# Kernel optimization log

Hardware: AMD Instinct MI355X
Metric: run time of the kernel (lower is better)

The kernel has to match this reference:

```python
import jax, jax.numpy as jnp
import numpy as np

DECAY = 0.99
EPS = 1e-12  # torch F.normalize eps


def setup_inputs() -> dict:
    key = jax.random.key(0)
    ks = jax.random.split(key, 5)
    B, S, H, M = 4, 4096, 1024, 256
    x = jax.random.normal(ks[0], (B, S, H), dtype=jnp.float32)
    Wq = jax.random.normal(ks[1], (M, H), dtype=jnp.float32) * (H ** -0.5)
    Wk = jax.random.normal(ks[2], (M, H), dtype=jnp.float32) * (H ** -0.5)
    Wv = jax.random.normal(ks[3], (M, H), dtype=jnp.float32) * (H ** -0.5)
    # original inits W_out to zeros; use small random weights so the baseline output is non-trivial
    Wo = jax.random.normal(ks[4], (H, M), dtype=jnp.float32) * (M ** -0.5)
    M0 = jnp.zeros((M, M), dtype=jnp.float32)
    return {"x": x, "Wq": Wq, "Wk": Wk, "Wv": Wv, "Wo": Wo, "M0": M0, "chunk_size": 64}


def _l2norm(t):
    return t / jnp.maximum(jnp.linalg.norm(t, axis=-1, keepdims=True), EPS)


def reference(x, Wq, Wk, Wv, Wo, M0, chunk_size):
    B, S, H = x.shape
    m = Wq.shape[0]
    q = jnp.einsum('bsh,mh->bsm', x, Wq)
    k = _l2norm(jnp.einsum('bsh,mh->bsm', x, Wk))
    v = _l2norm(jnp.einsum('bsh,mh->bsm', x, Wv))
    n_chunks = S // chunk_size
    # (n_chunks, B, c, m)
    qc = q.reshape(B, n_chunks, chunk_size, m).transpose(1, 0, 2, 3)
    kc = k.reshape(B, n_chunks, chunk_size, m).transpose(1, 0, 2, 3)
    vc = v.reshape(B, n_chunks, chunk_size, m).transpose(1, 0, 2, 3)
    decay_c = DECAY ** chunk_size
    scale = 1.0 / (B * chunk_size)

    def step(M, qkv):
        qch, kch, vch = qkv
        r = jnp.einsum('bcm,nm->bcn', qch, M)  # q @ M.T
        outer = jnp.einsum('bci,bcj->ij', vch, kch) * scale
        return decay_c * M + outer, r

    _, rs = jax.lax.scan(step, M0, (qc, kc, vc))  # rs: (n_chunks, B, c, m)
    retrieved = rs.transpose(1, 0, 2, 3).reshape(B, S, m)
    return jnp.einsum('bsm,hm->bsh', retrieved, Wo)
```

## Files before the change

### kernel.cpp

```cpp
#include <hip/hip_runtime.h>
#include <math.h>

#define BB 4
#define SS 4096
#define HH 1024
#define MM 256
#define CHUNK 64
#define NCHUNK 64
#define ROWS (BB*SS)
#define QKV_LD 768
#define DECAY_F 0.99

typedef unsigned short u16;
typedef __attribute__((ext_vector_type(8))) short bf16x8;
typedef __attribute__((ext_vector_type(8))) unsigned short u16x8;
typedef __attribute__((ext_vector_type(4))) float f32x4;

__device__ inline u16 f2b(float f) {
  union { float f; unsigned u; } v; v.f = f;
  unsigned r = v.u + 0x7FFF + ((v.u >> 16) & 1);
  return (u16)(r >> 16);
}
__device__ inline float b2f(u16 h) {
  union { unsigned u; float f; } v; v.u = ((unsigned)h) << 16; return v.f;
}

__device__ inline void gload16(const void* g, void* l) {
  __builtin_amdgcn_global_load_lds(
      (const __attribute__((address_space(1))) unsigned int*)g,
      (__attribute__((address_space(3))) unsigned int*)l, 16, 0, 0);
}

__global__ __launch_bounds__(256) void cast_x_kernel(const float* __restrict__ src,
                                                     u16* __restrict__ dst) {
  int i = blockIdx.x * 256 + threadIdx.x;
  float4 v = reinterpret_cast<const float4*>(src)[i];
  ushort4 o;
  o.x = f2b(v.x); o.y = f2b(v.y); o.z = f2b(v.z); o.w = f2b(v.w);
  reinterpret_cast<ushort4*>(dst)[i] = o;
}

__global__ __launch_bounds__(256) void cast_w_kernel(const float* __restrict__ Wq,
                                                     const float* __restrict__ Wk,
                                                     const float* __restrict__ Wv,
                                                     const float* __restrict__ Wo,
                                                     u16* __restrict__ Wqkv_b,
                                                     u16* __restrict__ Wo_b) {
  int b = blockIdx.x, which = b >> 8;
  int i = ((b & 255) << 8) + threadIdx.x;
  const float* src = which == 0 ? Wq : which == 1 ? Wk : which == 2 ? Wv : Wo;
  u16* dst = which < 3 ? Wqkv_b + which * (MM * HH) : Wo_b;
  float4 v = reinterpret_cast<const float4*>(src)[i];
  ushort4 o;
  o.x = f2b(v.x); o.y = f2b(v.y); o.z = f2b(v.z); o.w = f2b(v.w);
  reinterpret_cast<ushort4*>(dst)[i] = o;
}

template<int OUT_BF16>
__global__ __launch_bounds__(512, 2) void gemm256(const u16* __restrict__ A,
                                                  const u16* __restrict__ B,
                                                  void* __restrict__ Cv,
                                                  int K, int lda, int ldb, int ldc) {
  __shared__ bf16x8 LD[2][2][2][16][64];
  const int tid = threadIdx.x, lane = tid & 63, wv = tid >> 6;
  const int wr = wv >> 2, wc = wv & 3;

  const int gx = gridDim.x;
  const int nwg = gx * gridDim.y;
  const int lin = blockIdx.y * gx + blockIdx.x;
  const int chunk = nwg >> 3;
  const int orig = (lin & 7) * chunk + (lin >> 3);
  const int bx = orig % gx, by = orig / gx;
  const int row0 = by * 256, col0 = bx * 256;
  const int NT = K >> 6;

  const int fr = lane & 15;
  const int kg = (lane >> 4) << 3;

  auto stage2 = [&](int kt, int db, int part) {
    const int ab = part >> 1;
    const int j = part & 1;
    const int tile = wv + (j << 3);
    const u16* base = ab ? B : A;
    const int ld = ab ? ldb : lda;
    const int rc0 = ab ? col0 : row0;
    const u16* g = base + (size_t)(rc0 + tile * 16 + fr) * ld + kt * 64 + kg;
    gload16(g,      &LD[db][ab][0][tile][0]);
    gload16(g + 32, &LD[db][ab][1][tile][0]);
  };

  bf16x8 aq[4][2], bq[4][2];
  auto readAquad = [&](int db, int h) {
#pragma unroll
    for (int i = 0; i < 4; ++i)
#pragma unroll
      for (int s = 0; s < 2; ++s)
        aq[i][s] = LD[db][0][s][wr * 8 + h * 4 + i][lane];
  };
  auto readB2 = [&](int db, int nh) {
#pragma unroll
    for (int j = 0; j < 2; ++j)
#pragma unroll
      for (int s = 0; s < 2; ++s)
        bq[nh * 2 + j][s] = LD[db][1][s][wc * 4 + nh * 2 + j][lane];
  };

  f32x4 acc[8][4] = {};
  auto cluster = [&](int h, int nh) {
#pragma unroll
    for (int i = 0; i < 4; ++i)
#pragma unroll
      for (int j = 0; j < 2; ++j)
#pragma unroll
        for (int s = 0; s < 2; ++s)
          acc[h * 4 + i][nh * 2 + j] = __builtin_amdgcn_mfma_f32_16x16x32_bf16(
              aq[i][s], bq[nh * 2 + j][s], acc[h * 4 + i][nh * 2 + j], 0, 0, 0);
  };

  stage2(0, 0, 0); stage2(0, 0, 1); stage2(0, 0, 2); stage2(0, 0, 3);

  for (int kt = 0; kt < NT; ++kt) {
    const int db = kt & 1;
    const bool pf = (kt + 1 < NT);
    if (pf) stage2(kt + 1, db ^ 1, 0);
    if (pf) asm volatile("s_waitcnt vmcnt(2)" ::: "memory");
    else    asm volatile("s_waitcnt vmcnt(0)" ::: "memory");
    __builtin_amdgcn_s_barrier();
    asm volatile("" ::: "memory");
    readAquad(db, 0);
    readB2(db, 0);
    __builtin_amdgcn_s_setprio(1); cluster(0, 0); __builtin_amdgcn_s_setprio(0);
    __builtin_amdgcn_s_barrier();
    readB2(db, 1);
    if (pf) stage2(kt + 1, db ^ 1, 1);
    __builtin_amdgcn_s_barrier();
    __builtin_amdgcn_s_setprio(1); cluster(0, 1); __builtin_amdgcn_s_setprio(0);
    __builtin_amdgcn_s_barrier();
    readAquad(db, 1);
    if (pf) stage2(kt + 1, db ^ 1, 2);
    __builtin_amdgcn_s_barrier();
    __builtin_amdgcn_s_setprio(1); cluster(1, 0); __builtin_amdgcn_s_setprio(0);
    __builtin_amdgcn_s_barrier();
    if (pf) stage2(kt + 1, db ^ 1, 3);
    __builtin_amdgcn_s_barrier();
    __builtin_amdgcn_s_setprio(1); cluster(1, 1); __builtin_amdgcn_s_setprio(0);
    __builtin_amdgcn_s_barrier();
  }

  const int r4 = (lane >> 4) << 2;
  const int cc = lane & 15;
#pragma unroll
  for (int mi = 0; mi < 8; ++mi)
#pragma unroll
    for (int nj = 0; nj < 4; ++nj)
#pragma unroll
      for (int r = 0; r < 4; ++r) {
        int lr = wr * 128 + mi * 16 + r4 + r;
        int lc = wc * 64 + nj * 16 + cc;
        float vv = acc[mi][nj][r];
        if (OUT_BF16) ((u16*)Cv)[(size_t)(row0 + lr) * ldc + col0 + lc] = f2b(vv);
        else          ((float*)Cv)[(size_t)(row0 + lr) * ldc + col0 + lc] = vv;
      }
}

#define M_OUTER 2
#define M_RETR  3

template<int MODE>
__global__ __launch_bounds__(256) void gemm128(const u16* __restrict__ A,
                                               const u16* __restrict__ Bg,
                                               void* __restrict__ Cv,
                                               int K, int lda, int ldb,
                                               float scale) {
  __shared__ bf16x8 As[3][512];
  __shared__ bf16x8 Bs[3][512];
  const int tid = threadIdx.x, lane = tid & 63, wv = tid >> 6;
  const int wr = wv >> 1, wc = wv & 1;
  const int t = blockIdx.z;
  const int bx = blockIdx.x, by = blockIdx.y;
  const int row0 = by * 128;
  const int col0 = bx * 128;
  const int NK = K >> 5;
  const u16* Bbase = (MODE == M_RETR) ? (Bg + (size_t)t * (MM * MM)) : Bg;

  auto stage = [&](int ks, int buf) {
    int koff;
    if (MODE == M_OUTER) koff = ((ks >> 1) << 12) + t * CHUNK + ((ks & 1) << 5);
    else                 koff = ks << 5;
#pragma unroll
    for (int j = 0; j < 2; ++j) {
      int m = j * 4 + wv;
      int rf = m * 16 + (lane & 15);
      size_t arow;
      if (MODE == M_RETR)
        arow = (size_t)(2 * by + (rf >> 6)) * SS + (size_t)t * CHUNK + (rf & 63);
      else
        arow = (size_t)(row0 + rf);
      const u16* ga = A + arow * (size_t)lda + koff + ((lane >> 4) << 3);
      gload16(ga, &As[buf][m * 64]);
      const u16* gb = Bbase + (size_t)(col0 + rf) * ldb + koff + ((lane >> 4) << 3);
      gload16(gb, &Bs[buf][m * 64]);
    }
  };

  f32x4 acc[4][4] = {};
  stage(0, 0);
  stage(1, 1);
  int rb = 0, sb = 2;
  for (int ks = 0; ks < NK; ++ks) {
    if (ks + 1 < NK) asm volatile("s_waitcnt vmcnt(4)" ::: "memory");
    else             asm volatile("s_waitcnt vmcnt(0)" ::: "memory");
    __builtin_amdgcn_s_barrier();
    asm volatile("" ::: "memory");
    if (ks + 2 < NK) stage(ks + 2, sb);
    bf16x8 af[4], bfr[4];
#pragma unroll
    for (int m = 0; m < 4; ++m) af[m] = As[rb][(wr * 4 + m) * 64 + lane];
#pragma unroll
    for (int n = 0; n < 4; ++n) bfr[n] = Bs[rb][(wc * 4 + n) * 64 + lane];
#pragma unroll
    for (int m = 0; m < 4; ++m)
#pragma unroll
      for (int n = 0; n < 4; ++n)
        acc[m][n] = __builtin_amdgcn_mfma_f32_16x16x32_bf16(af[m], bfr[n], acc[m][n], 0, 0, 0);
    rb = (rb == 2) ? 0 : rb + 1;
    sb = (sb == 2) ? 0 : sb + 1;
  }

  const int r4 = (lane >> 4) << 2;
  const int cc = lane & 15;
#pragma unroll
  for (int m = 0; m < 4; ++m)
#pragma unroll
    for (int n = 0; n < 4; ++n)
#pragma unroll
      for (int r = 0; r < 4; ++r) {
        int lr = wr * 64 + m * 16 + r4 + r;
        int lc = wc * 64 + n * 16 + cc;
        float vv = acc[m][n][r];
        if (MODE == M_OUTER) {
          ((float*)Cv)[(size_t)t * (MM * MM) + (size_t)(row0 + lr) * MM + col0 + lc] = vv * scale;
        } else {
          size_t rowg = (size_t)(2 * by + (lr >> 6)) * SS + (size_t)t * CHUNK + (lr & 63);
          ((u16*)Cv)[rowg * MM + col0 + lc] = f2b(vv);
        }
      }
}

__global__ __launch_bounds__(256) void l2normT_kernel(const u16* __restrict__ qkv,
                                                      u16* __restrict__ kT,
                                                      u16* __restrict__ vT) {
  __shared__ u16 T[256][72];
  __shared__ float ps[64][4];
  __shared__ float inv[64];
  const int tid = threadIdx.x;
  const int q = tid >> 6, rl = tid & 63;
  const int row0 = blockIdx.x * 64;
#pragma unroll 1
  for (int seg = 0; seg < 2; ++seg) {
    u16* dstT = seg ? vT : kT;
    const int segbase = 256 + seg * 256;
    float ss = 0.f;
#pragma unroll
    for (int i = 0; i < 8; ++i) {
      u16x8 v = *reinterpret_cast<const u16x8*>(
          qkv + (size_t)(row0 + rl) * QKV_LD + segbase + q * 64 + i * 8);
#pragma unroll
      for (int e = 0; e < 8; ++e) {
        float f = b2f(v[e]);
        ss += f * f;
        T[q * 64 + i * 8 + e][rl] = v[e];
      }
    }
    ps[rl][q] = ss;
    __syncthreads();
    if (tid < 64) {
      float s = ps[tid][0] + ps[tid][1] + ps[tid][2] + ps[tid][3];
      inv[tid] = 1.0f / fmaxf(sqrtf(s), 1e-12f);
    }
    __syncthreads();
#pragma unroll
    for (int p = 0; p < 8; ++p) {
      int c = p * 32 + q * 8 + (rl >> 3);
      int r0 = (rl & 7) * 8;
      u16x8 val = *reinterpret_cast<const u16x8*>(&T[c][r0]);
      u16x8 o;
#pragma unroll
      for (int e = 0; e < 8; ++e) o[e] = f2b(b2f(val[e]) * inv[r0 + e]);
      *reinterpret_cast<u16x8*>(dstT + (size_t)c * ROWS + row0 + r0) = o;
    }
    __syncthreads();
  }
}

__global__ __launch_bounds__(256) void prefix_kernel(const float* __restrict__ outer,
                                                     const float* __restrict__ M0,
                                                     u16* __restrict__ Mprev_b,
                                                     float decay_c) {
  int ij = blockIdx.x * 256 + threadIdx.x;
  float run = M0[ij];
  float pre[8];
#pragma unroll
  for (int d = 0; d < 8; ++d) pre[d] = outer[(size_t)d * (MM * MM) + ij];
#pragma unroll 1
  for (int tb = 0; tb < NCHUNK; tb += 8) {
#pragma unroll
    for (int d = 0; d < 8; ++d) {
      int tc = tb + d;
      float o = pre[d];
      if (tb + 8 < NCHUNK) pre[d] = outer[(size_t)(tc + 8) * (MM * MM) + ij];
      Mprev_b[(size_t)tc * (MM * MM) + ij] = f2b(run);
      run = decay_c * run + o;
    }
  }
}

extern "C" void kernel_launch(void* const* d_in, const int* in_sizes, int n_in,
                              void* d_out, int out_size, void* d_ws, size_t ws_size,
                              hipStream_t stream) {
  const float* x  = (const float*)d_in[0];
  const float* Wq = (const float*)d_in[1];
  const float* Wk = (const float*)d_in[2];
  const float* Wv = (const float*)d_in[3];
  const float* Wo = (const float*)d_in[4];
  const float* M0 = (const float*)d_in[5];
  float* out = (float*)d_out;

  char* ws = (char*)d_ws;
  u16*   xb      = (u16*)(ws);
  u16*   qkv_b   = (u16*)(ws + 33554432);
  u16*   Wqkv_b  = (u16*)(ws + 58720256);
  u16*   Wo_b    = (u16*)(ws + 60293120);
  u16*   kT      = (u16*)(ws);
  u16*   vT      = (u16*)(ws + 8388608);
  float* outer   = (float*)(ws + 16777216);
  u16*   Mprev_b = (u16*)(ws);
  u16*   r_b     = (u16*)(ws + 8388608);

  const float scale   = 1.0f / (BB * CHUNK);
  const float decay_c = (float)pow(DECAY_F, (double)CHUNK);
  dim3 blk(256), blk512(512);

  cast_x_kernel<<<(ROWS * HH / 4) / 256, blk, 0, stream>>>(x, xb);
  cast_w_kernel<<<1024, blk, 0, stream>>>(Wq, Wk, Wv, Wo, Wqkv_b, Wo_b);
  gemm256<1><<<dim3(QKV_LD / 256, ROWS / 256), blk512, 0, stream>>>(
      xb, Wqkv_b, qkv_b, HH, HH, HH, QKV_LD);
  l2normT_kernel<<<ROWS / 64, blk, 0, stream>>>(qkv_b, kT, vT);
  gemm128<M_OUTER><<<dim3(2, 2, NCHUNK), blk, 0, stream>>>(
      vT, kT, outer, MM, ROWS, ROWS, scale);
  prefix_kernel<<<(MM * MM) / 256, blk, 0, stream>>>(outer, M0, Mprev_b, decay_c);
  gemm128<M_RETR><<<dim3(2, 2, NCHUNK), blk, 0, stream>>>(
      qkv_b, Mprev_b, r_b, MM, QKV_LD, MM, 0.f);
  gemm256<0><<<dim3(HH / 256, ROWS / 256), blk512, 0, stream>>>(
      r_b, Wo_b, out, MM, MM, MM, HH);
}
```

Baseline: 140.5 us.

## Fuse fp32-to-bf16 cast of x into QKV GEMM A-tile loading

Removes the separate cast_x kernel and has the QKV GEMM read x in fp32, convert it to bf16 in registers and write it to LDS inside the pipelined main loop. The QKV GEMM tile also changes to 256x192 (12 B tiles, 4x64 grid), so the 768 output columns split over four blocks instead of three. This drops a full bf16 round trip of x through memory (write plus reread). In exchange A loads go through registers instead of direct-to-LDS, which adds VGPR pressure, and x is read as fp32 once per column block, now four times instead of three.

```diff
diff --git a/kernel.cpp b/kernel.cpp
--- a/kernel.cpp
+++ b/kernel.cpp
@@ -24,20 +24,17 @@
 __device__ inline float b2f(u16 h) {
   union { unsigned u; float f; } v; v.u = ((unsigned)h) << 16; return v.f;
 }
+__device__ inline u16x8 cvt8(float4 p, float4 q) {
+  u16x8 h;
+  h[0] = f2b(p.x); h[1] = f2b(p.y); h[2] = f2b(p.z); h[3] = f2b(p.w);
+  h[4] = f2b(q.x); h[5] = f2b(q.y); h[6] = f2b(q.z); h[7] = f2b(q.w);
+  return h;
+}
 
 __device__ inline void gload16(const void* g, void* l) {
   __builtin_amdgcn_global_load_lds(
       (const __attribute__((address_space(1))) unsigned int*)g,
       (__attribute__((address_space(3))) unsigned int*)l, 16, 0, 0);
-}
-
-__global__ __launch_bounds__(256) void cast_x_kernel(const float* __restrict__ src,
-                                                     u16* __restrict__ dst) {
-  int i = blockIdx.x * 256 + threadIdx.x;
-  float4 v = reinterpret_cast<const float4*>(src)[i];
-  ushort4 o;
-  o.x = f2b(v.x); o.y = f2b(v.y); o.z = f2b(v.z); o.w = f2b(v.w);
-  reinterpret_cast<ushort4*>(dst)[i] = o;
 }
 
 __global__ __launch_bounds__(256) void cast_w_kernel(const float* __restrict__ Wq,
@@ -56,14 +53,17 @@
   reinterpret_cast<ushort4*>(dst)[i] = o;
 }
 
-template<int OUT_BF16>
-__global__ __launch_bounds__(512, 2) void gemm256(const u16* __restrict__ A,
+template<int NBT, int A_F32, int OUT_BF16>
+__global__ __launch_bounds__(512, 2) void gemm256(const void* __restrict__ Ap,
                                                   const u16* __restrict__ B,
                                                   void* __restrict__ Cv,
                                                   int K, int lda, int ldb, int ldc) {
-  __shared__ bf16x8 LD[2][2][2][16][64];
+  constexpr int NFR = NBT / 4;
+  __shared__ bf16x8 LA[2][2][16][64];
+  __shared__ bf16x8 LB[2][2][NBT][64];
   const int tid = threadIdx.x, lane = tid & 63, wv = tid >> 6;
   const int wr = wv >> 2, wc = wv & 3;
+  const int wvm3 = wv % 3;
 
   const int gx = gridDim.x;
   const int nwg = gx * gridDim.y;
@@ -71,77 +71,111 @@
   const int chunk = nwg >> 3;
   const int orig = (lin & 7) * chunk + (lin >> 3);
   const int bx = orig % gx, by = orig / gx;
-  const int row0 = by * 256, col0 = bx * 256;
+  const int row0 = by * 256, col0 = bx * (NBT * 16);
   const int NT = K >> 6;
 
   const int fr = lane & 15;
   const int kg = (lane >> 4) << 3;
 
-  auto stage2 = [&](int kt, int db, int part) {
-    const int ab = part >> 1;
-    const int j = part & 1;
-    const int tile = wv + (j << 3);
-    const u16* base = ab ? B : A;
-    const int ld = ab ? ldb : lda;
-    const int rc0 = ab ? col0 : row0;
-    const u16* g = base + (size_t)(rc0 + tile * 16 + fr) * ld + kt * 64 + kg;
-    gload16(g,      &LD[db][ab][0][tile][0]);
-    gload16(g + 32, &LD[db][ab][1][tile][0]);
-  };
-
-  bf16x8 aq[4][2], bq[4][2];
-  auto readAquad = [&](int db, int h) {
+  auto stageB = [&](int kt, int db_, int tile) {
+    const u16* g = B + (size_t)(col0 + tile * 16 + fr) * (size_t)ldb + kt * 64 + kg;
+    gload16(g,      &LB[db_][0][tile][0]);
+    gload16(g + 32, &LB[db_][1][tile][0]);
+  };
+  auto stageA_lds = [&](int kt, int db_, int tile) {
+    const u16* g = (const u16*)Ap + (size_t)(row0 + tile * 16 + fr) * (size_t)lda + kt * 64 + kg;
+    gload16(g,      &LA[db_][0][tile][0]);
+    gload16(g + 32, &LA[db_][1][tile][0]);
+  };
+  auto loadA = [&](int kt, int tile, float4& p0, float4& p1, float4& p2, float4& p3) {
+    const float* g = (const float*)Ap + (size_t)(row0 + tile * 16 + fr) * (size_t)lda + kt * 64 + kg;
+    p0 = *(const float4*)g;        p1 = *(const float4*)(g + 4);
+    p2 = *(const float4*)(g + 32); p3 = *(const float4*)(g + 36);
+  };
+  auto writeA = [&](int db_, int tile, float4 p0, float4 p1, float4 p2, float4 p3) {
+    *reinterpret_cast<u16x8*>(&LA[db_][0][tile][lane]) = cvt8(p0, p1);
+    *reinterpret_cast<u16x8*>(&LA[db_][1][tile][lane]) = cvt8(p2, p3);
+  };
+
+  bf16x8 aq[4][2], bq[NFR][2];
+  auto readAquad = [&](int db_, int h) {
 #pragma unroll
     for (int i = 0; i < 4; ++i)
 #pragma unroll
       for (int s = 0; s < 2; ++s)
-        aq[i][s] = LD[db][0][s][wr * 8 + h * 4 + i][lane];
-  };
-  auto readB2 = [&](int db, int nh) {
-#pragma unroll
-    for (int j = 0; j < 2; ++j)
+        aq[i][s] = LA[db_][s][wr * 8 + h * 4 + i][lane];
+  };
+  auto readBhalf = [&](int db_, int half) {
+    const int n0 = half ? 2 : 0, n1 = half ? NFR : 2;
+#pragma unroll
+    for (int n = n0; n < n1; ++n)
 #pragma unroll
       for (int s = 0; s < 2; ++s)
-        bq[nh * 2 + j][s] = LD[db][1][s][wc * 4 + nh * 2 + j][lane];
-  };
-
-  f32x4 acc[8][4] = {};
-  auto cluster = [&](int h, int nh) {
+        bq[n][s] = LB[db_][s][wc * NFR + n][lane];
+  };
+
+  f32x4 acc[8][NFR] = {};
+  auto cluster = [&](int h, int half) {
+    const int n0 = half ? 2 : 0, n1 = half ? NFR : 2;
 #pragma unroll
     for (int i = 0; i < 4; ++i)
 #pragma unroll
-      for (int j = 0; j < 2; ++j)
+      for (int n = n0; n < n1; ++n)
 #pragma unroll
         for (int s = 0; s < 2; ++s)
-          acc[h * 4 + i][nh * 2 + j] = __builtin_amdgcn_mfma_f32_16x16x32_bf16(
-              aq[i][s], bq[nh * 2 + j][s], acc[h * 4 + i][nh * 2 + j], 0, 0, 0);
-  };
-
-  stage2(0, 0, 0); stage2(0, 0, 1); stage2(0, 0, 2); stage2(0, 0, 3);
+          acc[h * 4 + i][n] = __builtin_amdgcn_mfma_f32_16x16x32_bf16(
+              aq[i][s], bq[n][s], acc[h * 4 + i][n], 0, 0, 0);
+  };
+
+  float4 pA0, pA1, pA2, pA3, pB0, pB1, pB2, pB3;
+
+  if constexpr (A_F32) {
+    stageB(0, 0, 0 + wvm3); stageB(0, 0, 3 + wvm3);
+    stageB(0, 0, 6 + wvm3); stageB(0, 0, 9 + wvm3);
+    loadA(0, wv,     pA0, pA1, pA2, pA3);
+    writeA(0, wv,    pA0, pA1, pA2, pA3);
+    loadA(0, wv + 8, pB0, pB1, pB2, pB3);
+    writeA(0, wv + 8, pB0, pB1, pB2, pB3);
+    asm volatile("s_waitcnt lgkmcnt(0)" ::: "memory");
+  } else {
+    stageA_lds(0, 0, wv); stageA_lds(0, 0, wv + 8);
+    stageB(0, 0, wv);     stageB(0, 0, wv + 8);
+  }
 
   for (int kt = 0; kt < NT; ++kt) {
-    const int db = kt & 1;
+    const int db = kt & 1, sb = db ^ 1;
     const bool pf = (kt + 1 < NT);
-    if (pf) stage2(kt + 1, db ^ 1, 0);
+    if (pf) { if constexpr (A_F32) stageB(kt + 1, sb, 0 + wvm3); else stageA_lds(kt + 1, sb, wv); }
     if (pf) asm volatile("s_waitcnt vmcnt(2)" ::: "memory");
     else    asm volatile("s_waitcnt vmcnt(0)" ::: "memory");
     __builtin_amdgcn_s_barrier();
     asm volatile("" ::: "memory");
     readAquad(db, 0);
-    readB2(db, 0);
+    readBhalf(db, 0);
     __builtin_amdgcn_s_setprio(1); cluster(0, 0); __builtin_amdgcn_s_setprio(0);
     __builtin_amdgcn_s_barrier();
-    readB2(db, 1);
-    if (pf) stage2(kt + 1, db ^ 1, 1);
+    readBhalf(db, 1);
+    if (pf) { if constexpr (A_F32) stageB(kt + 1, sb, 3 + wvm3); else stageA_lds(kt + 1, sb, wv + 8); }
     __builtin_amdgcn_s_barrier();
     __builtin_amdgcn_s_setprio(1); cluster(0, 1); __builtin_amdgcn_s_setprio(0);
     __builtin_amdgcn_s_barrier();
     readAquad(db, 1);
-    if (pf) stage2(kt + 1, db ^ 1, 2);
+    if (pf) {
+      if constexpr (A_F32) { loadA(kt + 1, wv, pA0, pA1, pA2, pA3); stageB(kt + 1, sb, 6 + wvm3); }
+      else stageB(kt + 1, sb, wv);
+    }
     __builtin_amdgcn_s_barrier();
     __builtin_amdgcn_s_setprio(1); cluster(1, 0); __builtin_amdgcn_s_setprio(0);
     __builtin_amdgcn_s_barrier();
-    if (pf) stage2(kt + 1, db ^ 1, 3);
+    if (pf) {
+      if constexpr (A_F32) {
+        writeA(sb, wv, pA0, pA1, pA2, pA3);
+        loadA(kt + 1, wv + 8, pB0, pB1, pB2, pB3);
+        stageB(kt + 1, sb, 9 + wvm3);
+        writeA(sb, wv + 8, pB0, pB1, pB2, pB3);
+        asm volatile("s_waitcnt lgkmcnt(0)" ::: "memory");
+      } else stageB(kt + 1, sb, wv + 8);
+    }
     __builtin_amdgcn_s_barrier();
     __builtin_amdgcn_s_setprio(1); cluster(1, 1); __builtin_amdgcn_s_setprio(0);
     __builtin_amdgcn_s_barrier();
@@ -152,11 +186,11 @@
 #pragma unroll
   for (int mi = 0; mi < 8; ++mi)
 #pragma unroll
-    for (int nj = 0; nj < 4; ++nj)
+    for (int nj = 0; nj < NFR; ++nj)
 #pragma unroll
       for (int r = 0; r < 4; ++r) {
         int lr = wr * 128 + mi * 16 + r4 + r;
-        int lc = wc * 64 + nj * 16 + cc;
+        int lc = wc * (NFR * 16) + nj * 16 + cc;
         float vv = acc[mi][nj][r];
         if (OUT_BF16) ((u16*)Cv)[(size_t)(row0 + lr) * ldc + col0 + lc] = f2b(vv);
         else          ((float*)Cv)[(size_t)(row0 + lr) * ldc + col0 + lc] = vv;
@@ -327,30 +361,28 @@
   float* out = (float*)d_out;
 
   char* ws = (char*)d_ws;
-  u16*   xb      = (u16*)(ws);
-  u16*   qkv_b   = (u16*)(ws + 33554432);
+  u16*   qkv_b   = (u16*)(ws);
+  u16*   kT      = (u16*)(ws + 25165824);
+  u16*   vT      = (u16*)(ws + 33554432);
+  float* outer   = (float*)(ws + 41943040);
+  u16*   Mprev_b = (u16*)(ws + 25165824);
+  u16*   r_b     = (u16*)(ws + 33554432);
   u16*   Wqkv_b  = (u16*)(ws + 58720256);
   u16*   Wo_b    = (u16*)(ws + 60293120);
-  u16*   kT      = (u16*)(ws);
-  u16*   vT      = (u16*)(ws + 8388608);
-  float* outer   = (float*)(ws + 16777216);
-  u16*   Mprev_b = (u16*)(ws);
-  u16*   r_b     = (u16*)(ws + 8388608);
 
   const float scale   = 1.0f / (BB * CHUNK);
   const float decay_c = (float)pow(DECAY_F, (double)CHUNK);
   dim3 blk(256), blk512(512);
 
-  cast_x_kernel<<<(ROWS * HH / 4) / 256, blk, 0, stream>>>(x, xb);
   cast_w_kernel<<<1024, blk, 0, stream>>>(Wq, Wk, Wv, Wo, Wqkv_b, Wo_b);
-  gemm256<1><<<dim3(QKV_LD / 256, ROWS / 256), blk512, 0, stream>>>(
-      xb, Wqkv_b, qkv_b, HH, HH, HH, QKV_LD);
+  gemm256<12, 1, 1><<<dim3(4, 64), blk512, 0, stream>>>(
+      x, Wqkv_b, qkv_b, HH, HH, HH, QKV_LD);
   l2normT_kernel<<<ROWS / 64, blk, 0, stream>>>(qkv_b, kT, vT);
   gemm128<M_OUTER><<<dim3(2, 2, NCHUNK), blk, 0, stream>>>(
       vT, kT, outer, MM, ROWS, ROWS, scale);
   prefix_kernel<<<(MM * MM) / 256, blk, 0, stream>>>(outer, M0, Mprev_b, decay_c);
   gemm128<M_RETR><<<dim3(2, 2, NCHUNK), blk, 0, stream>>>(
       qkv_b, Mprev_b, r_b, MM, QKV_LD, MM, 0.f);
-  gemm256<0><<<dim3(HH / 256, ROWS / 256), blk512, 0, stream>>>(
+  gemm256<16, 0, 0><<<dim3(4, 64), blk512, 0, stream>>>(
       r_b, Wo_b, out, MM, MM, MM, HH);
 }
```

Measured after the change: 164.1 us. 16.8% more time.

## Simplify GEMM pipeline to one barrier per k-tile with bulk prefetch

Applied to the files above, without the earlier changes.

Replaces the interleaved eight-barrier ping-pong schedule in the bf16 GEMM with a simpler loop. Each k-tile now waits for all loads, takes one barrier, issues every prefetch for the next tile, then reads all of B and A and runs the MFMA clusters back to back. This removes most barriers and the fine-grained staging. The trade-off is that global loads no longer interleave as tightly with compute, and the full vmcnt(0) wait can expose memory latency.

```diff
diff --git a/kernel.cpp b/kernel.cpp
--- a/kernel.cpp
+++ b/kernel.cpp
@@ -61,7 +61,8 @@
                                                   const u16* __restrict__ B,
                                                   void* __restrict__ Cv,
                                                   int K, int lda, int ldb, int ldc) {
-  __shared__ bf16x8 LD[2][2][2][16][64];
+  __shared__ bf16x8 LA[2][2][16][64];
+  __shared__ bf16x8 LB[2][2][16][64];
   const int tid = threadIdx.x, lane = tid & 63, wv = tid >> 6;
   const int wr = wv >> 2, wc = wv & 3;
 
@@ -77,32 +78,31 @@
   const int fr = lane & 15;
   const int kg = (lane >> 4) << 3;
 
-  auto stage2 = [&](int kt, int db, int part) {
-    const int ab = part >> 1;
-    const int j = part & 1;
-    const int tile = wv + (j << 3);
-    const u16* base = ab ? B : A;
-    const int ld = ab ? ldb : lda;
-    const int rc0 = ab ? col0 : row0;
-    const u16* g = base + (size_t)(rc0 + tile * 16 + fr) * ld + kt * 64 + kg;
-    gload16(g,      &LD[db][ab][0][tile][0]);
-    gload16(g + 32, &LD[db][ab][1][tile][0]);
+  auto stageA = [&](int kt, int db_, int tile) {
+    const u16* g = A + (size_t)(row0 + tile * 16 + fr) * (size_t)lda + kt * 64 + kg;
+    gload16(g,      &LA[db_][0][tile][0]);
+    gload16(g + 32, &LA[db_][1][tile][0]);
+  };
+  auto stageB = [&](int kt, int db_, int tile) {
+    const u16* g = B + (size_t)(col0 + tile * 16 + fr) * (size_t)ldb + kt * 64 + kg;
+    gload16(g,      &LB[db_][0][tile][0]);
+    gload16(g + 32, &LB[db_][1][tile][0]);
   };
 
   bf16x8 aq[4][2], bq[4][2];
-  auto readAquad = [&](int db, int h) {
+  auto readAquad = [&](int db_, int h) {
 #pragma unroll
     for (int i = 0; i < 4; ++i)
 #pragma unroll
       for (int s = 0; s < 2; ++s)
-        aq[i][s] = LD[db][0][s][wr * 8 + h * 4 + i][lane];
-  };
-  auto readB2 = [&](int db, int nh) {
-#pragma unroll
-    for (int j = 0; j < 2; ++j)
+        aq[i][s] = LA[db_][s][wr * 8 + h * 4 + i][lane];
+  };
+  auto readBall = [&](int db_) {
+#pragma unroll
+    for (int n = 0; n < 4; ++n)
 #pragma unroll
       for (int s = 0; s < 2; ++s)
-        bq[nh * 2 + j][s] = LD[db][1][s][wc * 4 + nh * 2 + j][lane];
+        bq[n][s] = LB[db_][s][wc * 4 + n][lane];
   };
 
   f32x4 acc[8][4] = {};
@@ -117,34 +117,27 @@
               aq[i][s], bq[nh * 2 + j][s], acc[h * 4 + i][nh * 2 + j], 0, 0, 0);
   };
 
-  stage2(0, 0, 0); stage2(0, 0, 1); stage2(0, 0, 2); stage2(0, 0, 3);
+  stageA(0, 0, wv); stageA(0, 0, wv + 8);
+  stageB(0, 0, wv); stageB(0, 0, wv + 8);
 
   for (int kt = 0; kt < NT; ++kt) {
-    const int db = kt & 1;
-    const bool pf = (kt + 1 < NT);
-    if (pf) stage2(kt + 1, db ^ 1, 0);
-    if (pf) asm volatile("s_waitcnt vmcnt(2)" ::: "memory");
-    else    asm volatile("s_waitcnt vmcnt(0)" ::: "memory");
+    const int db = kt & 1, sb = db ^ 1;
+    asm volatile("s_waitcnt vmcnt(0)" ::: "memory");
     __builtin_amdgcn_s_barrier();
     asm volatile("" ::: "memory");
+    if (kt + 1 < NT) {
+      stageA(kt + 1, sb, wv); stageA(kt + 1, sb, wv + 8);
+      stageB(kt + 1, sb, wv); stageB(kt + 1, sb, wv + 8);
+    }
     readAquad(db, 0);
-    readB2(db, 0);
-    __builtin_amdgcn_s_setprio(1); cluster(0, 0); __builtin_amdgcn_s_setprio(0);
-    __builtin_amdgcn_s_barrier();
-    readB2(db, 1);
-    if (pf) stage2(kt + 1, db ^ 1, 1);
-    __builtin_amdgcn_s_barrier();
-    __builtin_amdgcn_s_setprio(1); cluster(0, 1); __builtin_amdgcn_s_setprio(0);
-    __builtin_amdgcn_s_barrier();
+    readBall(db);
+    __builtin_amdgcn_s_setprio(1);
+    cluster(0, 0); cluster(0, 1);
+    __builtin_amdgcn_s_setprio(0);
     readAquad(db, 1);
-    if (pf) stage2(kt + 1, db ^ 1, 2);
-    __builtin_amdgcn_s_barrier();
-    __builtin_amdgcn_s_setprio(1); cluster(1, 0); __builtin_amdgcn_s_setprio(0);
-    __builtin_amdgcn_s_barrier();
-    if (pf) stage2(kt + 1, db ^ 1, 3);
-    __builtin_amdgcn_s_barrier();
-    __builtin_amdgcn_s_setprio(1); cluster(1, 1); __builtin_amdgcn_s_setprio(0);
-    __builtin_amdgcn_s_barrier();
+    __builtin_amdgcn_s_setprio(1);
+    cluster(1, 0); cluster(1, 1);
+    __builtin_amdgcn_s_setprio(0);
   }
 
   const int r4 = (lane >> 4) << 2;
```

Result: slower. 151.1 us (+7.6%).

## Fuse L2-normalize and transpose into QKV GEMM epilogue; merge cast kernels

Applied to the files above, without the earlier changes.

The QKV projection GEMM epilogue now writes q row-major and, for the k and v column tiles, computes row L2 norms by shuffle and shared-memory reduction, then writes normalized transposed kT/vT directly. This removes the separate l2normT kernel and the round trip of k and v through a bf16 qkv buffer. The two cast kernels are merged into one launch. The transposed epilogue stores are 8-byte strided writes, which may coalesce poorly, and the workspace layout is rearranged.

```diff
diff --git a/kernel.cpp b/kernel.cpp
--- a/kernel.cpp
+++ b/kernel.cpp
@@ -8,7 +8,6 @@
 #define CHUNK 64
 #define NCHUNK 64
 #define ROWS (BB*SS)
-#define QKV_LD 768
 #define DECAY_F 0.99
 
 typedef unsigned short u16;
@@ -31,35 +30,38 @@
       (__attribute__((address_space(3))) unsigned int*)l, 16, 0, 0);
 }
 
-__global__ __launch_bounds__(256) void cast_x_kernel(const float* __restrict__ src,
-                                                     u16* __restrict__ dst) {
-  int i = blockIdx.x * 256 + threadIdx.x;
+__global__ __launch_bounds__(256) void cast_all_kernel(const float* __restrict__ x,
+                                                       const float* __restrict__ Wq,
+                                                       const float* __restrict__ Wk,
+                                                       const float* __restrict__ Wv,
+                                                       const float* __restrict__ Wo,
+                                                       u16* __restrict__ xb,
+                                                       u16* __restrict__ Wqkv_b,
+                                                       u16* __restrict__ Wo_b) {
+  int b = blockIdx.x;
+  const float* src;
+  u16* dst;
+  int i;
+  if (b < 16384) {
+    src = x; dst = xb; i = (b << 8) + threadIdx.x;
+  } else {
+    int wb = b - 16384, which = wb >> 8;
+    i = ((wb & 255) << 8) + threadIdx.x;
+    src = which == 0 ? Wq : which == 1 ? Wk : which == 2 ? Wv : Wo;
+    dst = which < 3 ? Wqkv_b + which * (MM * HH) : Wo_b;
+  }
   float4 v = reinterpret_cast<const float4*>(src)[i];
   ushort4 o;
   o.x = f2b(v.x); o.y = f2b(v.y); o.z = f2b(v.z); o.w = f2b(v.w);
   reinterpret_cast<ushort4*>(dst)[i] = o;
 }
 
-__global__ __launch_bounds__(256) void cast_w_kernel(const float* __restrict__ Wq,
-                                                     const float* __restrict__ Wk,
-                                                     const float* __restrict__ Wv,
-                                                     const float* __restrict__ Wo,
-                                                     u16* __restrict__ Wqkv_b,
-                                                     u16* __restrict__ Wo_b) {
-  int b = blockIdx.x, which = b >> 8;
-  int i = ((b & 255) << 8) + threadIdx.x;
-  const float* src = which == 0 ? Wq : which == 1 ? Wk : which == 2 ? Wv : Wo;
-  u16* dst = which < 3 ? Wqkv_b + which * (MM * HH) : Wo_b;
-  float4 v = reinterpret_cast<const float4*>(src)[i];
-  ushort4 o;
-  o.x = f2b(v.x); o.y = f2b(v.y); o.z = f2b(v.z); o.w = f2b(v.w);
-  reinterpret_cast<ushort4*>(dst)[i] = o;
-}
-
-template<int OUT_BF16>
+template<int EPI>
 __global__ __launch_bounds__(512, 2) void gemm256(const u16* __restrict__ A,
                                                   const u16* __restrict__ B,
                                                   void* __restrict__ Cv,
+                                                  u16* __restrict__ kTd,
+                                                  u16* __restrict__ vTd,
                                                   int K, int lda, int ldb, int ldc) {
   __shared__ bf16x8 LD[2][2][2][16][64];
   const int tid = threadIdx.x, lane = tid & 63, wv = tid >> 6;
@@ -149,18 +151,76 @@
 
   const int r4 = (lane >> 4) << 2;
   const int cc = lane & 15;
-#pragma unroll
-  for (int mi = 0; mi < 8; ++mi)
-#pragma unroll
-    for (int nj = 0; nj < 4; ++nj)
-#pragma unroll
-      for (int r = 0; r < 4; ++r) {
-        int lr = wr * 128 + mi * 16 + r4 + r;
-        int lc = wc * 64 + nj * 16 + cc;
-        float vv = acc[mi][nj][r];
-        if (OUT_BF16) ((u16*)Cv)[(size_t)(row0 + lr) * ldc + col0 + lc] = f2b(vv);
-        else          ((float*)Cv)[(size_t)(row0 + lr) * ldc + col0 + lc] = vv;
+
+  if constexpr (EPI == 0) {
+#pragma unroll
+    for (int mi = 0; mi < 8; ++mi)
+#pragma unroll
+      for (int nj = 0; nj < 4; ++nj)
+#pragma unroll
+        for (int r = 0; r < 4; ++r) {
+          int lr = wr * 128 + mi * 16 + r4 + r;
+          int lc = wc * 64 + nj * 16 + cc;
+          ((float*)Cv)[(size_t)(row0 + lr) * ldc + col0 + lc] = acc[mi][nj][r];
+        }
+  } else {
+    if (bx == 0) {
+#pragma unroll
+      for (int mi = 0; mi < 8; ++mi)
+#pragma unroll
+        for (int nj = 0; nj < 4; ++nj)
+#pragma unroll
+          for (int r = 0; r < 4; ++r) {
+            int lr = wr * 128 + mi * 16 + r4 + r;
+            int lc = wc * 64 + nj * 16 + cc;
+            ((u16*)Cv)[(size_t)(row0 + lr) * MM + lc] = f2b(acc[mi][nj][r]);
+          }
+    } else {
+      u16* dstT = (bx == 1) ? kTd : vTd;
+      __syncthreads();
+      float* ps = reinterpret_cast<float*>(&LD[0][0][0][0][0]);
+#pragma unroll
+      for (int mi = 0; mi < 8; ++mi)
+#pragma unroll
+        for (int r = 0; r < 4; ++r) {
+          float p = 0.f;
+#pragma unroll
+          for (int nj = 0; nj < 4; ++nj) {
+            float v = acc[mi][nj][r];
+            p += v * v;
+          }
+          p += __shfl_xor(p, 1);
+          p += __shfl_xor(p, 2);
+          p += __shfl_xor(p, 4);
+          p += __shfl_xor(p, 8);
+          if (cc == 0)
+            ps[(wr * 128 + mi * 16 + (lane >> 4) * 4 + r) * 4 + wc] = p;
+        }
+      __syncthreads();
+#pragma unroll
+      for (int mi = 0; mi < 8; ++mi) {
+        int rowb = wr * 128 + mi * 16 + r4;
+        float4 s0 = *reinterpret_cast<float4*>(&ps[(rowb + 0) * 4]);
+        float4 s1 = *reinterpret_cast<float4*>(&ps[(rowb + 1) * 4]);
+        float4 s2 = *reinterpret_cast<float4*>(&ps[(rowb + 2) * 4]);
+        float4 s3 = *reinterpret_cast<float4*>(&ps[(rowb + 3) * 4]);
+        float iv0 = 1.0f / fmaxf(sqrtf(s0.x + s0.y + s0.z + s0.w), 1e-12f);
+        float iv1 = 1.0f / fmaxf(sqrtf(s1.x + s1.y + s1.z + s1.w), 1e-12f);
+        float iv2 = 1.0f / fmaxf(sqrtf(s2.x + s2.y + s2.z + s2.w), 1e-12f);
+        float iv3 = 1.0f / fmaxf(sqrtf(s3.x + s3.y + s3.z + s3.w), 1e-12f);
+#pragma unroll
+        for (int nj = 0; nj < 4; ++nj) {
+          int col = wc * 64 + nj * 16 + cc;
+          ushort4 o;
+          o.x = f2b(acc[mi][nj][0] * iv0);
+          o.y = f2b(acc[mi][nj][1] * iv1);
+          o.z = f2b(acc[mi][nj][2] * iv2);
+          o.w = f2b(acc[mi][nj][3] * iv3);
+          *reinterpret_cast<ushort4*>(&dstT[(size_t)col * ROWS + row0 + rowb]) = o;
+        }
       }
+    }
+  }
 }
 
 #define M_OUTER 2
@@ -247,52 +307,6 @@
       }
 }
 
-__global__ __launch_bounds__(256) void l2normT_kernel(const u16* __restrict__ qkv,
-                                                      u16* __restrict__ kT,
-                                                      u16* __restrict__ vT) {
-  __shared__ u16 T[256][72];
-  __shared__ float ps[64][4];
-  __shared__ float inv[64];
-  const int tid = threadIdx.x;
-  const int q = tid >> 6, rl = tid & 63;
-  const int row0 = blockIdx.x * 64;
-#pragma unroll 1
-  for (int seg = 0; seg < 2; ++seg) {
-    u16* dstT = seg ? vT : kT;
-    const int segbase = 256 + seg * 256;
-    float ss = 0.f;
-#pragma unroll
-    for (int i = 0; i < 8; ++i) {
-      u16x8 v = *reinterpret_cast<const u16x8*>(
-          qkv + (size_t)(row0 + rl) * QKV_LD + segbase + q * 64 + i * 8);
-#pragma unroll
-      for (int e = 0; e < 8; ++e) {
-        float f = b2f(v[e]);
-        ss += f * f;
-        T[q * 64 + i * 8 + e][rl] = v[e];
-      }
-    }
-    ps[rl][q] = ss;
-    __syncthreads();
-    if (tid < 64) {
-      float s = ps[tid][0] + ps[tid][1] + ps[tid][2] + ps[tid][3];
-      inv[tid] = 1.0f / fmaxf(sqrtf(s), 1e-12f);
-    }
-    __syncthreads();
-#pragma unroll
-    for (int p = 0; p < 8; ++p) {
-      int c = p * 32 + q * 8 + (rl >> 3);
-      int r0 = (rl & 7) * 8;
-      u16x8 val = *reinterpret_cast<const u16x8*>(&T[c][r0]);
-      u16x8 o;
-#pragma unroll
-      for (int e = 0; e < 8; ++e) o[e] = f2b(b2f(val[e]) * inv[r0 + e]);
-      *reinterpret_cast<u16x8*>(dstT + (size_t)c * ROWS + row0 + r0) = o;
-    }
-    __syncthreads();
-  }
-}
-
 __global__ __launch_bounds__(256) void prefix_kernel(const float* __restrict__ outer,
                                                      const float* __restrict__ M0,
                                                      u16* __restrict__ Mprev_b,
@@ -328,29 +342,28 @@
 
   char* ws = (char*)d_ws;
   u16*   xb      = (u16*)(ws);
-  u16*   qkv_b   = (u16*)(ws + 33554432);
+  u16*   q_b     = (u16*)(ws + 33554432);
+  u16*   kT      = (u16*)(ws + 41943040);
+  u16*   vT      = (u16*)(ws + 50331648);
   u16*   Wqkv_b  = (u16*)(ws + 58720256);
   u16*   Wo_b    = (u16*)(ws + 60293120);
-  u16*   kT      = (u16*)(ws);
-  u16*   vT      = (u16*)(ws + 8388608);
-  float* outer   = (float*)(ws + 16777216);
-  u16*   Mprev_b = (u16*)(ws);
-  u16*   r_b     = (u16*)(ws + 8388608);
+  float* outer   = (float*)(ws);
+  u16*   Mprev_b = (u16*)(ws + 16777216);
+  u16*   r_b     = (u16*)(ws + 41943040);
 
   const float scale   = 1.0f / (BB * CHUNK);
   const float decay_c = (float)pow(DECAY_F, (double)CHUNK);
   dim3 blk(256), blk512(512);
 
-  cast_x_kernel<<<(ROWS * HH / 4) / 256, blk, 0, stream>>>(x, xb);
-  cast_w_kernel<<<1024, blk, 0, stream>>>(Wq, Wk, Wv, Wo, Wqkv_b, Wo_b);
-  gemm256<1><<<dim3(QKV_LD / 256, ROWS / 256), blk512, 0, stream>>>(
-      xb, Wqkv_b, qkv_b, HH, HH, HH, QKV_LD);
-  l2normT_kernel<<<ROWS / 64, blk, 0, stream>>>(qkv_b, kT, vT);
+  cast_all_kernel<<<16384 + 1024, blk, 0, stream>>>(x, Wq, Wk, Wv, Wo,
+                                                    xb, Wqkv_b, Wo_b);
+  gemm256<2><<<dim3(3, ROWS / 256), blk512, 0, stream>>>(
+      xb, Wqkv_b, q_b, kT, vT, HH, HH, HH, MM);
   gemm128<M_OUTER><<<dim3(2, 2, NCHUNK), blk, 0, stream>>>(
       vT, kT, outer, MM, ROWS, ROWS, scale);
   prefix_kernel<<<(MM * MM) / 256, blk, 0, stream>>>(outer, M0, Mprev_b, decay_c);
   gemm128<M_RETR><<<dim3(2, 2, NCHUNK), blk, 0, stream>>>(
-      qkv_b, Mprev_b, r_b, MM, QKV_LD, MM, 0.f);
+      q_b, Mprev_b, r_b, MM, MM, MM, 0.f);
   gemm256<0><<<dim3(HH / 256, ROWS / 256), blk512, 0, stream>>>(
-      r_b, Wo_b, out, MM, MM, MM, HH);
-}
+      r_b, Wo_b, out, nullptr, nullptr, MM, MM, MM, HH);
+}
```

After: 134.4 us, median of 2. 1.05x faster.
